# Kernel tuning notes

Measured on AMD Instinct MI355X. Metric: run time of the kernel, lower is better.

The kernel has to match this reference:

```python
import jax, jax.numpy as jnp
import numpy as np

N = 4096      # batch (e.g. nodes)
MUL = 128     # multiplicity of every irrep chunk
INV_SQRT3 = 1.0 / float(np.sqrt(3.0))  # CG norm for 1x1->0 and 0x1->1 / 1x0->1
INV_SQRT6 = 1.0 / float(np.sqrt(6.0))  # CG norm for 1x1->1 (Levi-Civita / sqrt(6))

# Levi-Civita tensor eps[i,j,k]
_EPS = np.zeros((3, 3, 3), dtype=np.float32)
for a, b, c in [(0, 1, 2), (1, 2, 0), (2, 0, 1)]:
    _EPS[a, b, c] = 1.0
    _EPS[a, c, b] = -1.0
EPS = jnp.asarray(_EPS)


def setup_inputs() -> dict:
    key = jax.random.key(0)
    ks = jax.random.split(key, 9)
    # e3nn path normalization folded into weight init std:
    # std = 1/sqrt(mul1*mul2*num_paths_into_that_output_irrep)
    std2 = 1.0 / float(np.sqrt(MUL * MUL * 2))  # scalar out: 2 paths
    std3 = 1.0 / float(np.sqrt(MUL * MUL * 3))  # vector out: 3 paths
    W = (MUL, MUL, MUL)
    return {
        "x1_s": jax.random.normal(ks[0], (N, MUL), dtype=jnp.float32),
        "x1_v": jax.random.normal(ks[1], (N, MUL, 3), dtype=jnp.float32),
        "x2_s": jax.random.normal(ks[2], (N, MUL), dtype=jnp.float32),
        "x2_v": jax.random.normal(ks[3], (N, MUL, 3), dtype=jnp.float32),
        "w_sss": jax.random.normal(ks[4], W, dtype=jnp.float32) * std2,
        "w_vvs": jax.random.normal(ks[5], W, dtype=jnp.float32) * std2,
        "w_svv": jax.random.normal(ks[6], W, dtype=jnp.float32) * std3,
        "w_vsv": jax.random.normal(ks[7], W, dtype=jnp.float32) * std3,
        "w_vvv": jax.random.normal(ks[8], W, dtype=jnp.float32) * std3,
    }


def reference(x1_s, x1_v, x2_s, x2_v, w_sss, w_vvs, w_svv, w_vsv, w_vvv):
    # ---- paths into 0e (scalar) output ----
    # 0e x 0e -> 0e : CG = 1
    a = jnp.einsum('nu,uvw->nvw', x1_s, w_sss)           # [N,MUL,MUL]
    out_s = jnp.einsum('nvw,nv->nw', a, x2_s)            # [N,MUL]
    # 1o x 1o -> 0e : CG = delta_ij / sqrt(3)
    dot = jnp.einsum('nui,nvi->nuv', x1_v, x2_v) * INV_SQRT3
    out_s = out_s + jnp.einsum('nuv,uvw->nw', dot, w_vvs)
    # ---- paths into 1o (vector) output ----
    # 0e x 1o -> 1o : CG = delta / sqrt(3)
    b = jnp.einsum('nu,uvw->nvw', x1_s, w_svv)
    out_v = jnp.einsum('nvw,nvk->nwk', b, x2_v) * INV_SQRT3   # [N,MUL,3]
    # 1o x 0e -> 1o : CG = delta / sqrt(3)
    c = jnp.einsum('nv,uvw->nuw', x2_s, w_vsv)
    out_v = out_v + jnp.einsum('nuw,nuk->nwk', c, x1_v) * INV_SQRT3
    # 1o x 1o -> 1o : CG = eps_ijk / sqrt(6)  (cross product)
    c1 = jnp.einsum('nvj,ijk->nvik', x2_v, EPS)               # [N,MUL,3,3]
    cross = jnp.einsum('nui,nvik->nuvk', x1_v, c1)            # [N,MUL,MUL,3]
    out_v = out_v + jnp.einsum('nuvk,uvw->nwk', cross, w_vvv) * INV_SQRT6
    # pack IrrepsArray 128x0e+128x1o as flat [N, 128 + 384]
    return jnp.concatenate([out_s, out_v.reshape(out_v.shape[0], -1)], axis=-1)
```

## Files before the change

### kernel.cpp

```cpp
#include <hip/hip_runtime.h>
#include <hip/hip_bf16.h>


typedef _Float16 f16;
typedef _Float16 f16x8 __attribute__((ext_vector_type(8)));
typedef _Float16 h2 __attribute__((ext_vector_type(2)));
typedef float f32x4 __attribute__((ext_vector_type(4)));
typedef unsigned u32;

#define WT_BYTES  (5u*4u*128u*4096u*2u)
#define X1_BYTES  (64u*4u*8192u*2u)
#define SLICE_EL  1310720u
#define CHUNK_EL  10240u

__device__ __forceinline__ h2 bc(u32 x){ union{u32 u; h2 h;} c; c.u=x; return c.h; }

union F8 { h2 h[4]; f16x8 v; };

__device__ __forceinline__ void gl_lds16(const f16* g, f16* l) {
    __builtin_amdgcn_global_load_lds(
        (const __attribute__((address_space(1))) void*)g,
        (__attribute__((address_space(3))) void*)l,
        16, 0, 0);
}

__global__ __launch_bounds__(256) void pack_w_kernel(
    const float* __restrict__ w0, const float* __restrict__ w1,
    const float* __restrict__ w2, const float* __restrict__ w3,
    const float* __restrict__ w4, f16* __restrict__ wt)
{
    __shared__ float tl[64][130];
    const int b = blockIdx.x;
    const int p = b >> 7;
    const int u = b & 127;
    const int usec = u >> 5;
    const int uin  = u & 31;
    const float* src = (p==0)?w0:(p==1)?w1:(p==2)?w2:(p==3)?w3:w4;
    const float scale = (p==0)?1.0f:(p==4)?0.40824829046386302f:0.57735026918962576f;

    for (int h = 0; h < 2; ++h) {
        const float* spR = src + (size_t)u*16384 + (size_t)h*8192;
        #pragma unroll
        for (int k = 0; k < 8; ++k) {
            const int e4 = (k*256 + threadIdx.x) * 4;
            const float4 v4 = *(const float4*)(spR + e4);
            const int vi = e4 >> 7, w = e4 & 127;
            tl[vi][w+0]=v4.x; tl[vi][w+1]=v4.y; tl[vi][w+2]=v4.z; tl[vi][w+3]=v4.w;
        }
        __syncthreads();
        #pragma unroll
        for (int k = 0; k < 4; ++k) {
            const int cid = k*256 + threadIdx.x;
            const int q     = cid & 3;
            const int wg    = (cid >> 2) & 127;
            const int vbh   = cid >> 9;
            const int vb    = h*2 + vbh;
            const int c     = vb*32 + uin;
            const int whalf = wg >> 6;
            const int wl    = wg & 63;
            const int qs    = q ^ ((wl >> 1) & 3);
            f16x8 t8;
            #pragma unroll
            for (int j = 0; j < 8; ++j)
                t8[j] = (f16)(tl[vbh*32 + q*8 + j][wg] * scale);
            *(f16x8*)(wt + (size_t)(usec*2 + whalf)*SLICE_EL + (size_t)c*CHUNK_EL
                          + p*2048 + wl*32 + qs*8) = t8;
        }
        __syncthreads();
    }
}

__global__ __launch_bounds__(256) void pack_x_kernel(
    const float* __restrict__ x1s, const float* __restrict__ x1v,
    const float* __restrict__ x2s, const float* __restrict__ x2v,
    f16* __restrict__ x1g, f16* __restrict__ x2g)
{
    if (blockIdx.x < 128) {
        __shared__ uint2 tl[128][33];
        const int nb = blockIdx.x;
        #pragma unroll
        for (int k = 0; k < 16; ++k) {
            const int idx = k*256 + threadIdx.x;
            const int u = idx & 127, nd = idx >> 7;
            const size_t i = (size_t)(nb*32 + nd)*128 + u;
            union { f16 h[4]; uint2 u2; } tp;
            tp.h[0] = (f16)x1s[i];
            tp.h[1] = (f16)x1v[i*3 + 0];
            tp.h[2] = (f16)x1v[i*3 + 1];
            tp.h[3] = (f16)x1v[i*3 + 2];
            tl[u][nd] = tp.u2;
        }
        __syncthreads();
        uint2* og = (uint2*)x1g;
        const int t = nb >> 1, nd0 = (nb & 1) * 32;
        #pragma unroll
        for (int k = 0; k < 16; ++k) {
            const int idx = k*256 + threadIdx.x;
            const int u = idx >> 5, nd = idx & 31;
            og[(((t*4 + (u>>5))*32 + (u&31)) << 6) + nd0 + nd] = tl[u][nd];
        }
    } else {
        const int tt = (blockIdx.x - 128)*256 + threadIdx.x;
        const int n = tt >> 7, v = tt & 127;
        const size_t b = (size_t)n*512;
        const size_t i = (size_t)n*128 + v;
        x2g[b +   0 + v] = (f16)x2s[i];
        x2g[b + 128 + v] = (f16)x2v[i*3 + 0];
        x2g[b + 256 + v] = (f16)x2v[i*3 + 1];
        x2g[b + 384 + v] = (f16)x2v[i*3 + 2];
    }
}

__global__ __launch_bounds__(256, 2) void tp_main(
    const f16* __restrict__ wt, const f16* __restrict__ x1g,
    const f16* __restrict__ x2g, float* __restrict__ out)
{
    __shared__ __align__(16) f16 wlds[2*CHUNK_EL];
    __shared__ __align__(16) f16 x1lds[8192];

    const int tid  = threadIdx.x;
    const int lane = tid & 63;
    const int wv   = tid >> 6;
    const int kg   = lane >> 4;
    const int lr   = lane & 15;

    const int b     = blockIdx.x;
    const int slice = b & 7;
    const int t     = b >> 3;
    const int usec  = slice >> 1;
    const int whalf = slice & 1;

    const f16* wstream = wt + (size_t)slice * SLICE_EL;

    int boff[4];
    #pragma unroll
    for (int ct = 0; ct < 4; ++ct) {
        const int wp = ct*16 + lr;
        boff[ct] = wp*32 + ((kg ^ ((wp >> 1) & 3)) * 8);
    }

    {
        const f16* src = x1g + ((size_t)(t*4 + usec) << 13);
        #pragma unroll
        for (int r = 0; r < 4; ++r)
            gl_lds16(src + r*2048 + wv*512 + lane*8, x1lds + r*2048 + wv*512 + lane*8);
    }
    #pragma unroll
    for (int r = 0; r < 5; ++r)
        gl_lds16(wstream + r*2048 + wv*512 + lane*8, wlds + r*2048 + wv*512 + lane*8);

    f32x4 acc[4][4];
    #pragma unroll
    for (int c2 = 0; c2 < 4; ++c2)
        #pragma unroll
        for (int d = 0; d < 4; ++d)
            acc[c2][d] = (f32x4){0.f, 0.f, 0.f, 0.f};

    h2 xq[4][4];
    const f16* wsrc = wstream + CHUNK_EL + wv*512 + lane*8;
    const f16* x2base = x2g + ((size_t)(t*64 + wv*16 + lr) << 9) + kg*8;
    const int nodel4 = (wv*16 + lr) * 4;

    for (int vb = 0; vb < 4; ++vb) {
        {
            const f16* xb = x2base + vb*32;
            uint4 h0 = *(const uint4*)(xb);
            uint4 h1 = *(const uint4*)(xb + 128);
            uint4 h2v = *(const uint4*)(xb + 256);
            uint4 h3 = *(const uint4*)(xb + 384);
            xq[0][0]=bc(h0.x); xq[0][1]=bc(h0.y); xq[0][2]=bc(h0.z); xq[0][3]=bc(h0.w);
            xq[1][0]=bc(h1.x); xq[1][1]=bc(h1.y); xq[1][2]=bc(h1.z); xq[1][3]=bc(h1.w);
            xq[2][0]=bc(h2v.x); xq[2][1]=bc(h2v.y); xq[2][2]=bc(h2v.z); xq[2][3]=bc(h2v.w);
            xq[3][0]=bc(h3.x); xq[3][1]=bc(h3.y); xq[3][2]=bc(h3.z); xq[3][3]=bc(h3.w);
        }
        for (int u2b = 0; u2b < 32; u2b += 2) {
            #pragma unroll
            for (int uu = 0; uu < 2; ++uu) {
                const int u2 = u2b + uu;
                const int c  = vb*32 + u2;

                asm volatile("s_waitcnt vmcnt(0)" ::: "memory");
                __builtin_amdgcn_s_barrier();
                __builtin_amdgcn_sched_barrier(0);

                if (c < 127) {
                    f16* dc = wlds + (uu^1)*CHUNK_EL + wv*512;
                    #pragma unroll
                    for (int r = 0; r < 5; ++r)
                        gl_lds16(wsrc + r*2048, dc + r*2048 + lane*8);
                }
                wsrc += CHUNK_EL;

                const uint2 h1 = *(const uint2*)(x1lds + u2*256 + nodel4);
                const h2 ps1 = bc(__builtin_amdgcn_perm(h1.x, h1.x, 0x01000100u));
                h2 pv[3];
                pv[0] = bc(__builtin_amdgcn_perm(h1.x, h1.x, 0x03020302u));
                pv[1] = bc(__builtin_amdgcn_perm(h1.y, h1.y, 0x01000100u));
                pv[2] = bc(__builtin_amdgcn_perm(h1.y, h1.y, 0x03020302u));

                F8 f0, f1, fa[3], fb[3], fc[3];
                #pragma unroll
                for (int j = 0; j < 4; ++j) {
                    f0.h[j] = ps1 * xq[0][j];
                    h2 d = pv[0] * xq[1][j];
                    d = __builtin_elementwise_fma(pv[1], xq[2][j], d);
                    f1.h[j] = __builtin_elementwise_fma(pv[2], xq[3][j], d);
                }
                #pragma unroll
                for (int k = 0; k < 3; ++k) {
                    const int k1 = (k+1) % 3, k2 = (k+2) % 3;
                    #pragma unroll
                    for (int j = 0; j < 4; ++j) {
                        fa[k].h[j] = ps1   * xq[1+k][j];
                        fb[k].h[j] = pv[k] * xq[0][j];
                        h2 tx = pv[k1] * xq[1+k2][j];
                        fc[k].h[j] = __builtin_elementwise_fma(-pv[k2], xq[1+k1][j], tx);
                    }
                }

                const f16* wb = wlds + uu*CHUNK_EL;
                #pragma unroll
                for (int ct = 0; ct < 4; ++ct) {
                    f16x8 b0 = *(const f16x8*)(wb +    0 + boff[ct]);
                    f16x8 b1 = *(const f16x8*)(wb + 2048 + boff[ct]);
                    f16x8 b2 = *(const f16x8*)(wb + 4096 + boff[ct]);
                    f16x8 b3 = *(const f16x8*)(wb + 6144 + boff[ct]);
                    f16x8 b4 = *(const f16x8*)(wb + 8192 + boff[ct]);
                    acc[ct][0] = __builtin_amdgcn_mfma_f32_16x16x32_f16(f0.v, b0, acc[ct][0], 0,0,0);
                    acc[ct][0] = __builtin_amdgcn_mfma_f32_16x16x32_f16(f1.v, b1, acc[ct][0], 0,0,0);
                    #pragma unroll
                    for (int k = 0; k < 3; ++k) {
                        acc[ct][1+k] = __builtin_amdgcn_mfma_f32_16x16x32_f16(fa[k].v, b2, acc[ct][1+k], 0,0,0);
                        acc[ct][1+k] = __builtin_amdgcn_mfma_f32_16x16x32_f16(fb[k].v, b3, acc[ct][1+k], 0,0,0);
                        acc[ct][1+k] = __builtin_amdgcn_mfma_f32_16x16x32_f16(fc[k].v, b4, acc[ct][1+k], 0,0,0);
                    }
                }
            }
        }
    }

    #pragma unroll
    for (int ct = 0; ct < 4; ++ct) {
        const int w = whalf*64 + ct*16 + lr;
        #pragma unroll
        for (int j = 0; j < 4; ++j) {
            const int n = t*64 + wv*16 + kg*4 + j;
            float* op = out + (size_t)n*512;
            unsafeAtomicAdd(op + w,             acc[ct][0][j]);
            unsafeAtomicAdd(op + 128 + w*3 + 0, acc[ct][1][j]);
            unsafeAtomicAdd(op + 128 + w*3 + 1, acc[ct][2][j]);
            unsafeAtomicAdd(op + 128 + w*3 + 2, acc[ct][3][j]);
        }
    }
}

extern "C" void kernel_launch(void* const* d_in, const int* in_sizes, int n_in,
                              void* d_out, int out_size, void* d_ws, size_t ws_size,
                              hipStream_t stream)
{
    const float* x1s = (const float*)d_in[0];
    const float* x1v = (const float*)d_in[1];
    const float* x2s = (const float*)d_in[2];
    const float* x2v = (const float*)d_in[3];
    const float* w0  = (const float*)d_in[4];
    const float* w1  = (const float*)d_in[5];
    const float* w2  = (const float*)d_in[6];
    const float* w3  = (const float*)d_in[7];
    const float* w4  = (const float*)d_in[8];

    f16* wtb = (f16*)d_ws;
    f16* x1g = (f16*)((char*)d_ws + WT_BYTES);
    f16* x2g = (f16*)((char*)d_ws + WT_BYTES + X1_BYTES);
    float* out = (float*)d_out;

    pack_w_kernel<<<640, 256, 0, stream>>>(w0, w1, w2, w3, w4, wtb);
    pack_x_kernel<<<2176, 256, 0, stream>>>(x1s, x1v, x2s, x2v, x1g, x2g);
    hipMemsetAsync(d_out, 0, (size_t)out_size*sizeof(float), stream);
    tp_main<<<512, 256, 0, stream>>>(wtb, x1g, x2g, out);
}
```

Measured before the change: 234.1 us.

## Double node tile per block to reuse each weight chunk across two row tiles

Each block now processes 128 nodes (two 16-row MFMA tiles per wave) instead of 64, so every streamed weight chunk loaded into LDS feeds twice as many MFMAs. The grid halves to 256 blocks and the x1 packing layout is widened to match. Weight streaming traffic from global/L2 is halved, at the cost of doubled accumulator registers (launch bounds reduced to one block per SM) and fewer blocks, which lowers occupancy and latency hiding. On a 256-CU part the 256 blocks give roughly one block per CU.

```diff
diff --git a/kernel.cpp b/kernel.cpp
--- a/kernel.cpp
+++ b/kernel.cpp
@@ -9,7 +9,7 @@
 typedef unsigned u32;
 
 #define WT_BYTES  (5u*4u*128u*4096u*2u)
-#define X1_BYTES  (64u*4u*8192u*2u)
+#define X1_BYTES  (32u*4u*16384u*2u)
 #define SLICE_EL  1310720u
 #define CHUNK_EL  10240u
 
@@ -92,12 +92,12 @@
         }
         __syncthreads();
         uint2* og = (uint2*)x1g;
-        const int t = nb >> 1, nd0 = (nb & 1) * 32;
+        const int t = nb >> 2, nd0 = (nb & 3) * 32;
         #pragma unroll
         for (int k = 0; k < 16; ++k) {
             const int idx = k*256 + threadIdx.x;
             const int u = idx >> 5, nd = idx & 31;
-            og[(((t*4 + (u>>5))*32 + (u&31)) << 6) + nd0 + nd] = tl[u][nd];
+            og[(((t*4 + (u>>5))*32 + (u&31)) << 7) + nd0 + nd] = tl[u][nd];
         }
     } else {
         const int tt = (blockIdx.x - 128)*256 + threadIdx.x;
@@ -111,12 +111,12 @@
     }
 }
 
-__global__ __launch_bounds__(256, 2) void tp_main(
+__global__ __launch_bounds__(256, 1) void tp_main(
     const f16* __restrict__ wt, const f16* __restrict__ x1g,
     const f16* __restrict__ x2g, float* __restrict__ out)
 {
     __shared__ __align__(16) f16 wlds[2*CHUNK_EL];
-    __shared__ __align__(16) f16 x1lds[8192];
+    __shared__ __align__(16) f16 x1lds[16384];
 
     const int tid  = threadIdx.x;
     const int lane = tid & 63;
@@ -140,38 +140,41 @@
     }
 
     {
-        const f16* src = x1g + ((size_t)(t*4 + usec) << 13);
-        #pragma unroll
-        for (int r = 0; r < 4; ++r)
-            gl_lds16(src + r*2048 + wv*512 + lane*8, x1lds + r*2048 + wv*512 + lane*8);
+        const f16* src = x1g + ((size_t)(t*4 + usec) << 14);
+        #pragma unroll
+        for (int r = 0; r < 8; ++r)
+            gl_lds16(src + r*2048 + tid*8, x1lds + r*2048 + tid*8);
     }
     #pragma unroll
     for (int r = 0; r < 5; ++r)
-        gl_lds16(wstream + r*2048 + wv*512 + lane*8, wlds + r*2048 + wv*512 + lane*8);
-
-    f32x4 acc[4][4];
-    #pragma unroll
-    for (int c2 = 0; c2 < 4; ++c2)
-        #pragma unroll
-        for (int d = 0; d < 4; ++d)
-            acc[c2][d] = (f32x4){0.f, 0.f, 0.f, 0.f};
-
-    h2 xq[4][4];
-    const f16* wsrc = wstream + CHUNK_EL + wv*512 + lane*8;
-    const f16* x2base = x2g + ((size_t)(t*64 + wv*16 + lr) << 9) + kg*8;
-    const int nodel4 = (wv*16 + lr) * 4;
+        gl_lds16(wstream + r*2048 + tid*8, wlds + r*2048 + tid*8);
+    __syncthreads();
+
+    f32x4 acc[2][4][4];
+    #pragma unroll
+    for (int rt = 0; rt < 2; ++rt)
+        #pragma unroll
+        for (int c2 = 0; c2 < 4; ++c2)
+            #pragma unroll
+            for (int d = 0; d < 4; ++d)
+                acc[rt][c2][d] = (f32x4){0.f, 0.f, 0.f, 0.f};
+
+    h2 xq[2][4][4];
+    const f16* wsrc = wstream + CHUNK_EL + tid*8;
 
     for (int vb = 0; vb < 4; ++vb) {
-        {
-            const f16* xb = x2base + vb*32;
-            uint4 h0 = *(const uint4*)(xb);
-            uint4 h1 = *(const uint4*)(xb + 128);
-            uint4 h2v = *(const uint4*)(xb + 256);
-            uint4 h3 = *(const uint4*)(xb + 384);
-            xq[0][0]=bc(h0.x); xq[0][1]=bc(h0.y); xq[0][2]=bc(h0.z); xq[0][3]=bc(h0.w);
-            xq[1][0]=bc(h1.x); xq[1][1]=bc(h1.y); xq[1][2]=bc(h1.z); xq[1][3]=bc(h1.w);
-            xq[2][0]=bc(h2v.x); xq[2][1]=bc(h2v.y); xq[2][2]=bc(h2v.z); xq[2][3]=bc(h2v.w);
-            xq[3][0]=bc(h3.x); xq[3][1]=bc(h3.y); xq[3][2]=bc(h3.z); xq[3][3]=bc(h3.w);
+        #pragma unroll
+        for (int rt = 0; rt < 2; ++rt) {
+            const int n = t*128 + wv*32 + rt*16 + lr;
+            const f16* xb = x2g + ((size_t)n << 9) + kg*8 + vb*32;
+            const uint4 h0 = *(const uint4*)(xb);
+            const uint4 h1 = *(const uint4*)(xb + 128);
+            const uint4 h2v = *(const uint4*)(xb + 256);
+            const uint4 h3 = *(const uint4*)(xb + 384);
+            xq[rt][0][0]=bc(h0.x); xq[rt][0][1]=bc(h0.y); xq[rt][0][2]=bc(h0.z); xq[rt][0][3]=bc(h0.w);
+            xq[rt][1][0]=bc(h1.x); xq[rt][1][1]=bc(h1.y); xq[rt][1][2]=bc(h1.z); xq[rt][1][3]=bc(h1.w);
+            xq[rt][2][0]=bc(h2v.x); xq[rt][2][1]=bc(h2v.y); xq[rt][2][2]=bc(h2v.z); xq[rt][2][3]=bc(h2v.w);
+            xq[rt][3][0]=bc(h3.x); xq[rt][3][1]=bc(h3.y); xq[rt][3][2]=bc(h3.z); xq[rt][3][3]=bc(h3.w);
         }
         for (int u2b = 0; u2b < 32; u2b += 2) {
             #pragma unroll
@@ -184,55 +187,60 @@
                 __builtin_amdgcn_sched_barrier(0);
 
                 if (c < 127) {
-                    f16* dc = wlds + (uu^1)*CHUNK_EL + wv*512;
+                    f16* dc = wlds + (uu^1)*CHUNK_EL + tid*8;
                     #pragma unroll
                     for (int r = 0; r < 5; ++r)
-                        gl_lds16(wsrc + r*2048, dc + r*2048 + lane*8);
+                        gl_lds16(wsrc + r*2048, dc + r*2048);
                 }
                 wsrc += CHUNK_EL;
 
-                const uint2 h1 = *(const uint2*)(x1lds + u2*256 + nodel4);
-                const h2 ps1 = bc(__builtin_amdgcn_perm(h1.x, h1.x, 0x01000100u));
-                h2 pv[3];
-                pv[0] = bc(__builtin_amdgcn_perm(h1.x, h1.x, 0x03020302u));
-                pv[1] = bc(__builtin_amdgcn_perm(h1.y, h1.y, 0x01000100u));
-                pv[2] = bc(__builtin_amdgcn_perm(h1.y, h1.y, 0x03020302u));
-
-                F8 f0, f1, fa[3], fb[3], fc[3];
+                F8 ag[2][11];
                 #pragma unroll
-                for (int j = 0; j < 4; ++j) {
-                    f0.h[j] = ps1 * xq[0][j];
-                    h2 d = pv[0] * xq[1][j];
-                    d = __builtin_elementwise_fma(pv[1], xq[2][j], d);
-                    f1.h[j] = __builtin_elementwise_fma(pv[2], xq[3][j], d);
-                }
-                #pragma unroll
-                for (int k = 0; k < 3; ++k) {
-                    const int k1 = (k+1) % 3, k2 = (k+2) % 3;
+                for (int rt = 0; rt < 2; ++rt) {
+                    const uint2 h1 = *(const uint2*)(x1lds + u2*512 + (wv*32 + rt*16 + lr)*4);
+                    const h2 ps1 = bc(__builtin_amdgcn_perm(h1.x, h1.x, 0x01000100u));
+                    h2 pv[3];
+                    pv[0] = bc(__builtin_amdgcn_perm(h1.x, h1.x, 0x03020302u));
+                    pv[1] = bc(__builtin_amdgcn_perm(h1.y, h1.y, 0x01000100u));
+                    pv[2] = bc(__builtin_amdgcn_perm(h1.y, h1.y, 0x03020302u));
                     #pragma unroll
                     for (int j = 0; j < 4; ++j) {
-                        fa[k].h[j] = ps1   * xq[1+k][j];
-                        fb[k].h[j] = pv[k] * xq[0][j];
-                        h2 tx = pv[k1] * xq[1+k2][j];
-                        fc[k].h[j] = __builtin_elementwise_fma(-pv[k2], xq[1+k1][j], tx);
+                        ag[rt][0].h[j] = ps1 * xq[rt][0][j];
+                        h2 d = pv[0] * xq[rt][1][j];
+                        d = __builtin_elementwise_fma(pv[1], xq[rt][2][j], d);
+                        ag[rt][1].h[j] = __builtin_elementwise_fma(pv[2], xq[rt][3][j], d);
+                    }
+                    #pragma unroll
+                    for (int k = 0; k < 3; ++k) {
+                        const int k1 = (k+1) % 3, k2 = (k+2) % 3;
+                        #pragma unroll
+                        for (int j = 0; j < 4; ++j) {
+                            ag[rt][2+k].h[j] = ps1   * xq[rt][1+k][j];
+                            ag[rt][5+k].h[j] = pv[k] * xq[rt][0][j];
+                            h2 tx = pv[k1] * xq[rt][1+k2][j];
+                            ag[rt][8+k].h[j] = __builtin_elementwise_fma(-pv[k2], xq[rt][1+k1][j], tx);
+                        }
                     }
                 }
 
                 const f16* wb = wlds + uu*CHUNK_EL;
                 #pragma unroll
                 for (int ct = 0; ct < 4; ++ct) {
-                    f16x8 b0 = *(const f16x8*)(wb +    0 + boff[ct]);
-                    f16x8 b1 = *(const f16x8*)(wb + 2048 + boff[ct]);
-                    f16x8 b2 = *(const f16x8*)(wb + 4096 + boff[ct]);
-                    f16x8 b3 = *(const f16x8*)(wb + 6144 + boff[ct]);
-                    f16x8 b4 = *(const f16x8*)(wb + 8192 + boff[ct]);
-                    acc[ct][0] = __builtin_amdgcn_mfma_f32_16x16x32_f16(f0.v, b0, acc[ct][0], 0,0,0);
-                    acc[ct][0] = __builtin_amdgcn_mfma_f32_16x16x32_f16(f1.v, b1, acc[ct][0], 0,0,0);
-                    #pragma unroll
-                    for (int k = 0; k < 3; ++k) {
-                        acc[ct][1+k] = __builtin_amdgcn_mfma_f32_16x16x32_f16(fa[k].v, b2, acc[ct][1+k], 0,0,0);
-                        acc[ct][1+k] = __builtin_amdgcn_mfma_f32_16x16x32_f16(fb[k].v, b3, acc[ct][1+k], 0,0,0);
-                        acc[ct][1+k] = __builtin_amdgcn_mfma_f32_16x16x32_f16(fc[k].v, b4, acc[ct][1+k], 0,0,0);
+                    const f16x8 b0 = *(const f16x8*)(wb +    0 + boff[ct]);
+                    const f16x8 b1 = *(const f16x8*)(wb + 2048 + boff[ct]);
+                    const f16x8 b2 = *(const f16x8*)(wb + 4096 + boff[ct]);
+                    const f16x8 b3 = *(const f16x8*)(wb + 6144 + boff[ct]);
+                    const f16x8 b4 = *(const f16x8*)(wb + 8192 + boff[ct]);
+                    #pragma unroll
+                    for (int rt = 0; rt < 2; ++rt) {
+                        acc[rt][ct][0] = __builtin_amdgcn_mfma_f32_16x16x32_f16(ag[rt][0].v, b0, acc[rt][ct][0], 0,0,0);
+                        acc[rt][ct][0] = __builtin_amdgcn_mfma_f32_16x16x32_f16(ag[rt][1].v, b1, acc[rt][ct][0], 0,0,0);
+                        #pragma unroll
+                        for (int k = 0; k < 3; ++k) {
+                            acc[rt][ct][1+k] = __builtin_amdgcn_mfma_f32_16x16x32_f16(ag[rt][2+k].v, b2, acc[rt][ct][1+k], 0,0,0);
+                            acc[rt][ct][1+k] = __builtin_amdgcn_mfma_f32_16x16x32_f16(ag[rt][5+k].v, b3, acc[rt][ct][1+k], 0,0,0);
+                            acc[rt][ct][1+k] = __builtin_amdgcn_mfma_f32_16x16x32_f16(ag[rt][8+k].v, b4, acc[rt][ct][1+k], 0,0,0);
+                        }
                     }
                 }
             }
@@ -240,16 +248,19 @@
     }
 
     #pragma unroll
-    for (int ct = 0; ct < 4; ++ct) {
-        const int w = whalf*64 + ct*16 + lr;
-        #pragma unroll
-        for (int j = 0; j < 4; ++j) {
-            const int n = t*64 + wv*16 + kg*4 + j;
-            float* op = out + (size_t)n*512;
-            unsafeAtomicAdd(op + w,             acc[ct][0][j]);
-            unsafeAtomicAdd(op + 128 + w*3 + 0, acc[ct][1][j]);
-            unsafeAtomicAdd(op + 128 + w*3 + 1, acc[ct][2][j]);
-            unsafeAtomicAdd(op + 128 + w*3 + 2, acc[ct][3][j]);
+    for (int rt = 0; rt < 2; ++rt) {
+        #pragma unroll
+        for (int ct = 0; ct < 4; ++ct) {
+            const int w = whalf*64 + ct*16 + lr;
+            #pragma unroll
+            for (int j = 0; j < 4; ++j) {
+                const int n = t*128 + wv*32 + rt*16 + kg*4 + j;
+                float* op = out + (size_t)n*512;
+                unsafeAtomicAdd(op + w,             acc[rt][ct][0][j]);
+                unsafeAtomicAdd(op + 128 + w*3 + 0, acc[rt][ct][1][j]);
+                unsafeAtomicAdd(op + 128 + w*3 + 1, acc[rt][ct][2][j]);
+                unsafeAtomicAdd(op + 128 + w*3 + 2, acc[rt][ct][3][j]);
+            }
         }
     }
 }
@@ -276,5 +287,5 @@
     pack_w_kernel<<<640, 256, 0, stream>>>(w0, w1, w2, w3, w4, wtb);
     pack_x_kernel<<<2176, 256, 0, stream>>>(x1s, x1v, x2s, x2v, x1g, x2g);
     hipMemsetAsync(d_out, 0, (size_t)out_size*sizeof(float), stream);
-    tp_main<<<512, 256, 0, stream>>>(wtb, x1g, x2g, out);
-}
+    tp_main<<<256, 256, 0, stream>>>(wtb, x1g, x2g, out);
+}
```

Measured after the change: 267.3 us. 1.14x slower.

## Triple-buffer weight chunks in LDS with partial vmcnt waits and MFMA priority

Applied to the files above, without the earlier changes.

Moves the weight stream from a double buffer to a triple LDS buffer, prefetching two chunks ahead and waiting only on the older chunk's loads (vmcnt(5)) instead of draining all loads each step. It also raises wave priority around the MFMA block with s_setprio. LDS use grows by one chunk (about 20 KB), which may cut the occupancy of two blocks per CU. An extra __syncthreads is added after the initial loads.

```diff
diff --git a/kernel.cpp b/kernel.cpp
--- a/kernel.cpp
+++ b/kernel.cpp
@@ -115,7 +115,7 @@
     const f16* __restrict__ wt, const f16* __restrict__ x1g,
     const f16* __restrict__ x2g, float* __restrict__ out)
 {
-    __shared__ __align__(16) f16 wlds[2*CHUNK_EL];
+    __shared__ __align__(16) f16 wlds[3*CHUNK_EL];
     __shared__ __align__(16) f16 x1lds[8192];
 
     const int tid  = threadIdx.x;
@@ -146,8 +146,12 @@
             gl_lds16(src + r*2048 + wv*512 + lane*8, x1lds + r*2048 + wv*512 + lane*8);
     }
     #pragma unroll
-    for (int r = 0; r < 5; ++r)
-        gl_lds16(wstream + r*2048 + wv*512 + lane*8, wlds + r*2048 + wv*512 + lane*8);
+    for (int k = 0; k < 2; ++k)
+        #pragma unroll
+        for (int r = 0; r < 5; ++r)
+            gl_lds16(wstream + k*CHUNK_EL + r*2048 + tid*8,
+                     wlds    + k*CHUNK_EL + r*2048 + tid*8);
+    __syncthreads();
 
     f32x4 acc[4][4];
     #pragma unroll
@@ -157,87 +161,93 @@
             acc[c2][d] = (f32x4){0.f, 0.f, 0.f, 0.f};
 
     h2 xq[4][4];
-    const f16* wsrc = wstream + CHUNK_EL + wv*512 + lane*8;
+    const f16* wsrc = wstream + 2*CHUNK_EL + tid*8;
     const f16* x2base = x2g + ((size_t)(t*64 + wv*16 + lr) << 9) + kg*8;
     const int nodel4 = (wv*16 + lr) * 4;
 
-    for (int vb = 0; vb < 4; ++vb) {
-        {
-            const f16* xb = x2base + vb*32;
-            uint4 h0 = *(const uint4*)(xb);
-            uint4 h1 = *(const uint4*)(xb + 128);
-            uint4 h2v = *(const uint4*)(xb + 256);
-            uint4 h3 = *(const uint4*)(xb + 384);
+    auto body = [&](int c, int bi) __attribute__((always_inline)) {
+        if ((c & 31) == 0) {
+            const f16* xb = x2base + (c >> 5)*32;
+            const uint4 h0 = *(const uint4*)(xb);
+            const uint4 h1 = *(const uint4*)(xb + 128);
+            const uint4 h2v = *(const uint4*)(xb + 256);
+            const uint4 h3 = *(const uint4*)(xb + 384);
             xq[0][0]=bc(h0.x); xq[0][1]=bc(h0.y); xq[0][2]=bc(h0.z); xq[0][3]=bc(h0.w);
             xq[1][0]=bc(h1.x); xq[1][1]=bc(h1.y); xq[1][2]=bc(h1.z); xq[1][3]=bc(h1.w);
             xq[2][0]=bc(h2v.x); xq[2][1]=bc(h2v.y); xq[2][2]=bc(h2v.z); xq[2][3]=bc(h2v.w);
             xq[3][0]=bc(h3.x); xq[3][1]=bc(h3.y); xq[3][2]=bc(h3.z); xq[3][3]=bc(h3.w);
         }
-        for (int u2b = 0; u2b < 32; u2b += 2) {
-            #pragma unroll
-            for (int uu = 0; uu < 2; ++uu) {
-                const int u2 = u2b + uu;
-                const int c  = vb*32 + u2;
-
-                asm volatile("s_waitcnt vmcnt(0)" ::: "memory");
-                __builtin_amdgcn_s_barrier();
-                __builtin_amdgcn_sched_barrier(0);
-
-                if (c < 127) {
-                    f16* dc = wlds + (uu^1)*CHUNK_EL + wv*512;
-                    #pragma unroll
-                    for (int r = 0; r < 5; ++r)
-                        gl_lds16(wsrc + r*2048, dc + r*2048 + lane*8);
-                }
-                wsrc += CHUNK_EL;
-
-                const uint2 h1 = *(const uint2*)(x1lds + u2*256 + nodel4);
-                const h2 ps1 = bc(__builtin_amdgcn_perm(h1.x, h1.x, 0x01000100u));
-                h2 pv[3];
-                pv[0] = bc(__builtin_amdgcn_perm(h1.x, h1.x, 0x03020302u));
-                pv[1] = bc(__builtin_amdgcn_perm(h1.y, h1.y, 0x01000100u));
-                pv[2] = bc(__builtin_amdgcn_perm(h1.y, h1.y, 0x03020302u));
-
-                F8 f0, f1, fa[3], fb[3], fc[3];
-                #pragma unroll
-                for (int j = 0; j < 4; ++j) {
-                    f0.h[j] = ps1 * xq[0][j];
-                    h2 d = pv[0] * xq[1][j];
-                    d = __builtin_elementwise_fma(pv[1], xq[2][j], d);
-                    f1.h[j] = __builtin_elementwise_fma(pv[2], xq[3][j], d);
-                }
-                #pragma unroll
-                for (int k = 0; k < 3; ++k) {
-                    const int k1 = (k+1) % 3, k2 = (k+2) % 3;
-                    #pragma unroll
-                    for (int j = 0; j < 4; ++j) {
-                        fa[k].h[j] = ps1   * xq[1+k][j];
-                        fb[k].h[j] = pv[k] * xq[0][j];
-                        h2 tx = pv[k1] * xq[1+k2][j];
-                        fc[k].h[j] = __builtin_elementwise_fma(-pv[k2], xq[1+k1][j], tx);
-                    }
-                }
-
-                const f16* wb = wlds + uu*CHUNK_EL;
-                #pragma unroll
-                for (int ct = 0; ct < 4; ++ct) {
-                    f16x8 b0 = *(const f16x8*)(wb +    0 + boff[ct]);
-                    f16x8 b1 = *(const f16x8*)(wb + 2048 + boff[ct]);
-                    f16x8 b2 = *(const f16x8*)(wb + 4096 + boff[ct]);
-                    f16x8 b3 = *(const f16x8*)(wb + 6144 + boff[ct]);
-                    f16x8 b4 = *(const f16x8*)(wb + 8192 + boff[ct]);
-                    acc[ct][0] = __builtin_amdgcn_mfma_f32_16x16x32_f16(f0.v, b0, acc[ct][0], 0,0,0);
-                    acc[ct][0] = __builtin_amdgcn_mfma_f32_16x16x32_f16(f1.v, b1, acc[ct][0], 0,0,0);
-                    #pragma unroll
-                    for (int k = 0; k < 3; ++k) {
-                        acc[ct][1+k] = __builtin_amdgcn_mfma_f32_16x16x32_f16(fa[k].v, b2, acc[ct][1+k], 0,0,0);
-                        acc[ct][1+k] = __builtin_amdgcn_mfma_f32_16x16x32_f16(fb[k].v, b3, acc[ct][1+k], 0,0,0);
-                        acc[ct][1+k] = __builtin_amdgcn_mfma_f32_16x16x32_f16(fc[k].v, b4, acc[ct][1+k], 0,0,0);
-                    }
-                }
+
+        if (c < 127) { asm volatile("s_waitcnt vmcnt(5)" ::: "memory"); }
+        else         { asm volatile("s_waitcnt vmcnt(0)" ::: "memory"); }
+        __builtin_amdgcn_s_barrier();
+        __builtin_amdgcn_sched_barrier(0);
+
+        if (c < 126) {
+            f16* dc = wlds + ((bi + 2) % 3)*CHUNK_EL + tid*8;
+            #pragma unroll
+            for (int r = 0; r < 5; ++r)
+                gl_lds16(wsrc + r*2048, dc + r*2048);
+        }
+        wsrc += CHUNK_EL;
+
+        const int u2 = c & 31;
+
+        const uint2 h1 = *(const uint2*)(x1lds + u2*256 + nodel4);
+        const h2 ps1 = bc(__builtin_amdgcn_perm(h1.x, h1.x, 0x01000100u));
+        h2 pv[3];
+        pv[0] = bc(__builtin_amdgcn_perm(h1.x, h1.x, 0x03020302u));
+        pv[1] = bc(__builtin_amdgcn_perm(h1.y, h1.y, 0x01000100u));
+        pv[2] = bc(__builtin_amdgcn_perm(h1.y, h1.y, 0x03020302u));
+
+        F8 f0, f1, fa[3], fb[3], fc[3];
+        #pragma unroll
+        for (int j = 0; j < 4; ++j) {
+            f0.h[j] = ps1 * xq[0][j];
+            h2 d = pv[0] * xq[1][j];
+            d = __builtin_elementwise_fma(pv[1], xq[2][j], d);
+            f1.h[j] = __builtin_elementwise_fma(pv[2], xq[3][j], d);
+        }
+        #pragma unroll
+        for (int k = 0; k < 3; ++k) {
+            const int k1 = (k+1) % 3, k2 = (k+2) % 3;
+            #pragma unroll
+            for (int j = 0; j < 4; ++j) {
+                fa[k].h[j] = ps1   * xq[1+k][j];
+                fb[k].h[j] = pv[k] * xq[0][j];
+                h2 tx = pv[k1] * xq[1+k2][j];
+                fc[k].h[j] = __builtin_elementwise_fma(-pv[k2], xq[1+k1][j], tx);
             }
         }
-    }
+
+        const f16* wb = wlds + bi*CHUNK_EL;
+        __builtin_amdgcn_s_setprio(1);
+        #pragma unroll
+        for (int ct = 0; ct < 4; ++ct) {
+            const f16x8 b0 = *(const f16x8*)(wb +    0 + boff[ct]);
+            const f16x8 b1 = *(const f16x8*)(wb + 2048 + boff[ct]);
+            const f16x8 b2 = *(const f16x8*)(wb + 4096 + boff[ct]);
+            const f16x8 b3 = *(const f16x8*)(wb + 6144 + boff[ct]);
+            const f16x8 b4 = *(const f16x8*)(wb + 8192 + boff[ct]);
+            acc[ct][0] = __builtin_amdgcn_mfma_f32_16x16x32_f16(f0.v, b0, acc[ct][0], 0,0,0);
+            acc[ct][0] = __builtin_amdgcn_mfma_f32_16x16x32_f16(f1.v, b1, acc[ct][0], 0,0,0);
+            #pragma unroll
+            for (int k = 0; k < 3; ++k) {
+                acc[ct][1+k] = __builtin_amdgcn_mfma_f32_16x16x32_f16(fa[k].v, b2, acc[ct][1+k], 0,0,0);
+                acc[ct][1+k] = __builtin_amdgcn_mfma_f32_16x16x32_f16(fb[k].v, b3, acc[ct][1+k], 0,0,0);
+                acc[ct][1+k] = __builtin_amdgcn_mfma_f32_16x16x32_f16(fc[k].v, b4, acc[ct][1+k], 0,0,0);
+            }
+        }
+        __builtin_amdgcn_s_setprio(0);
+    };
+
+    for (int cb = 0; cb < 126; cb += 3) {
+        body(cb + 0, 0);
+        body(cb + 1, 1);
+        body(cb + 2, 2);
+    }
+    body(126, 0);
+    body(127, 1);
 
     #pragma unroll
     for (int ct = 0; ct < 4; ++ct) {
```

Measured after the change: 240.2 us. +2.6%, slower.

## Switch to 32x32x16 MFMA tiles and stream weights directly into registers

Applied to the files above, without the earlier changes.

Replaces the 16x16x32 MFMA tiling with 32x32x16 tiles covering 128 nodes per block. Each block now handles 16 u-values per slice, across 16 slices. The LDS double-buffered weight stream, with its per-chunk barriers, is dropped; B fragments are loaded from global memory into registers with one-step software prefetch. The aim is to remove the barrier and LDS round-trip overhead and to reuse each B load across more rows. The cost is much higher register pressure from the B10 buffers and f32x16 accumulators, more global load traffic, and changed weight/x1 pack layouts. The launch grid must match the new 16-slice mapping, and that part of the host code is not shown.

```diff
diff --git a/kernel.cpp b/kernel.cpp
--- a/kernel.cpp
+++ b/kernel.cpp
@@ -5,17 +5,18 @@
 typedef _Float16 f16;
 typedef _Float16 f16x8 __attribute__((ext_vector_type(8)));
 typedef _Float16 h2 __attribute__((ext_vector_type(2)));
-typedef float f32x4 __attribute__((ext_vector_type(4)));
+typedef float f32x16 __attribute__((ext_vector_type(16)));
 typedef unsigned u32;
 
 #define WT_BYTES  (5u*4u*128u*4096u*2u)
-#define X1_BYTES  (64u*4u*8192u*2u)
-#define SLICE_EL  1310720u
+#define X1_BYTES  (32u*8u*8192u*2u)
+#define SLICE_EL  655360u
 #define CHUNK_EL  10240u
 
 __device__ __forceinline__ h2 bc(u32 x){ union{u32 u; h2 h;} c; c.u=x; return c.h; }
 
 union F8 { h2 h[4]; f16x8 v; };
+struct B10 { f16x8 v[10]; };
 
 __device__ __forceinline__ void gl_lds16(const f16* g, f16* l) {
     __builtin_amdgcn_global_load_lds(
@@ -33,8 +34,8 @@
     const int b = blockIdx.x;
     const int p = b >> 7;
     const int u = b & 127;
-    const int usec = u >> 5;
-    const int uin  = u & 31;
+    const int usec = u >> 4;
+    const int uin  = u & 15;
     const float* src = (p==0)?w0:(p==1)?w1:(p==2)?w2:(p==3)?w3:w4;
     const float scale = (p==0)?1.0f:(p==4)?0.40824829046386302f:0.57735026918962576f;
 
@@ -55,16 +56,18 @@
             const int wg    = (cid >> 2) & 127;
             const int vbh   = cid >> 9;
             const int vb    = h*2 + vbh;
-            const int c     = vb*32 + uin;
+            const int c     = vb*16 + uin;
+            const int kb    = q >> 1;
+            const int h2i   = q & 1;
             const int whalf = wg >> 6;
             const int wl    = wg & 63;
-            const int qs    = q ^ ((wl >> 1) & 3);
+            const int s     = usec*2 + whalf;
             f16x8 t8;
             #pragma unroll
             for (int j = 0; j < 8; ++j)
                 t8[j] = (f16)(tl[vbh*32 + q*8 + j][wg] * scale);
-            *(f16x8*)(wt + (size_t)(usec*2 + whalf)*SLICE_EL + (size_t)c*CHUNK_EL
-                          + p*2048 + wl*32 + qs*8) = t8;
+            *(f16x8*)(wt + (size_t)s*SLICE_EL + (size_t)c*CHUNK_EL
+                          + p*2048 + kb*1024 + wl*16 + h2i*8) = t8;
         }
         __syncthreads();
     }
@@ -92,12 +95,12 @@
         }
         __syncthreads();
         uint2* og = (uint2*)x1g;
-        const int t = nb >> 1, nd0 = (nb & 1) * 32;
+        const int t = nb >> 2, nd0 = (nb & 3) * 32;
         #pragma unroll
         for (int k = 0; k < 16; ++k) {
             const int idx = k*256 + threadIdx.x;
             const int u = idx >> 5, nd = idx & 31;
-            og[(((t*4 + (u>>5))*32 + (u&31)) << 6) + nd0 + nd] = tl[u][nd];
+            og[(((t*8 + (u>>4))*16 + (u&15)) << 7) + nd0 + nd] = tl[u][nd];
         }
     } else {
         const int tt = (blockIdx.x - 128)*256 + threadIdx.x;
@@ -111,145 +114,137 @@
     }
 }
 
+__device__ __forceinline__ B10 loadB(const f16* cb, int kb, int bo){
+    B10 r;
+    #pragma unroll
+    for (int p = 0; p < 5; ++p)
+        #pragma unroll
+        for (int ct = 0; ct < 2; ++ct)
+            r.v[p*2+ct] = *(const f16x8*)(cb + p*2048 + kb*1024 + ct*512 + bo);
+    return r;
+}
+
 __global__ __launch_bounds__(256, 2) void tp_main(
     const f16* __restrict__ wt, const f16* __restrict__ x1g,
     const f16* __restrict__ x2g, float* __restrict__ out)
 {
-    __shared__ __align__(16) f16 wlds[2*CHUNK_EL];
     __shared__ __align__(16) f16 x1lds[8192];
 
     const int tid  = threadIdx.x;
     const int lane = tid & 63;
     const int wv   = tid >> 6;
-    const int kg   = lane >> 4;
-    const int lr   = lane & 15;
+    const int l5   = lane & 31;
+    const int kg2  = lane >> 5;
 
     const int b     = blockIdx.x;
-    const int slice = b & 7;
-    const int t     = b >> 3;
+    const int slice = b & 15;
+    const int t     = b >> 4;
     const int usec  = slice >> 1;
     const int whalf = slice & 1;
 
-    const f16* wstream = wt + (size_t)slice * SLICE_EL;
-
-    int boff[4];
+    const f16* wbase = wt + (size_t)slice * SLICE_EL;
+    const int bo = l5*16 + kg2*8;
+
+    {
+        const f16* src = x1g + (size_t)(t*8 + usec) * 8192;
+        #pragma unroll
+        for (int r = 0; r < 4; ++r)
+            gl_lds16(src + r*2048 + tid*8, x1lds + r*2048 + tid*8);
+    }
+    __syncthreads();
+
+    f32x16 acc[2][4];
     #pragma unroll
-    for (int ct = 0; ct < 4; ++ct) {
-        const int wp = ct*16 + lr;
-        boff[ct] = wp*32 + ((kg ^ ((wp >> 1) & 3)) * 8);
-    }
-
-    {
-        const f16* src = x1g + ((size_t)(t*4 + usec) << 13);
-        #pragma unroll
-        for (int r = 0; r < 4; ++r)
-            gl_lds16(src + r*2048 + wv*512 + lane*8, x1lds + r*2048 + wv*512 + lane*8);
-    }
-    #pragma unroll
-    for (int r = 0; r < 5; ++r)
-        gl_lds16(wstream + r*2048 + wv*512 + lane*8, wlds + r*2048 + wv*512 + lane*8);
-
-    f32x4 acc[4][4];
-    #pragma unroll
-    for (int c2 = 0; c2 < 4; ++c2)
-        #pragma unroll
-        for (int d = 0; d < 4; ++d)
-            acc[c2][d] = (f32x4){0.f, 0.f, 0.f, 0.f};
-
-    h2 xq[4][4];
-    const f16* wsrc = wstream + CHUNK_EL + wv*512 + lane*8;
-    const f16* x2base = x2g + ((size_t)(t*64 + wv*16 + lr) << 9) + kg*8;
-    const int nodel4 = (wv*16 + lr) * 4;
-
-    for (int vb = 0; vb < 4; ++vb) {
-        {
-            const f16* xb = x2base + vb*32;
-            uint4 h0 = *(const uint4*)(xb);
-            uint4 h1 = *(const uint4*)(xb + 128);
-            uint4 h2v = *(const uint4*)(xb + 256);
-            uint4 h3 = *(const uint4*)(xb + 384);
-            xq[0][0]=bc(h0.x); xq[0][1]=bc(h0.y); xq[0][2]=bc(h0.z); xq[0][3]=bc(h0.w);
-            xq[1][0]=bc(h1.x); xq[1][1]=bc(h1.y); xq[1][2]=bc(h1.z); xq[1][3]=bc(h1.w);
-            xq[2][0]=bc(h2v.x); xq[2][1]=bc(h2v.y); xq[2][2]=bc(h2v.z); xq[2][3]=bc(h2v.w);
-            xq[3][0]=bc(h3.x); xq[3][1]=bc(h3.y); xq[3][2]=bc(h3.z); xq[3][3]=bc(h3.w);
-        }
-        for (int u2b = 0; u2b < 32; u2b += 2) {
-            #pragma unroll
-            for (int uu = 0; uu < 2; ++uu) {
-                const int u2 = u2b + uu;
-                const int c  = vb*32 + u2;
-
-                asm volatile("s_waitcnt vmcnt(0)" ::: "memory");
-                __builtin_amdgcn_s_barrier();
-                __builtin_amdgcn_sched_barrier(0);
-
-                if (c < 127) {
-                    f16* dc = wlds + (uu^1)*CHUNK_EL + wv*512;
-                    #pragma unroll
-                    for (int r = 0; r < 5; ++r)
-                        gl_lds16(wsrc + r*2048, dc + r*2048 + lane*8);
+    for (int c2 = 0; c2 < 2; ++c2)
+        #pragma unroll
+        for (int ch = 0; ch < 4; ++ch)
+            #pragma unroll
+            for (int r = 0; r < 16; ++r)
+                acc[c2][ch][r] = 0.f;
+
+    h2 xq[4][2][4];
+    const int node = wv*32 + l5;
+    const f16* x2b = x2g + (size_t)(t*128 + node)*512 + kg2*8;
+
+    const f16* cb = wbase;
+    B10 B0 = loadB(cb, 0, bo);
+    uint2 h1c = *(const uint2*)(x1lds + node*4);
+
+    for (int c = 0; c < 64; ++c) {
+        const int vb = c >> 4, u = c & 15;
+        if (u == 0) {
+            #pragma unroll
+            for (int q = 0; q < 4; ++q)
+                #pragma unroll
+                for (int kb = 0; kb < 2; ++kb) {
+                    const uint4 hx = *(const uint4*)(x2b + q*128 + vb*32 + kb*16);
+                    xq[q][kb][0]=bc(hx.x); xq[q][kb][1]=bc(hx.y);
+                    xq[q][kb][2]=bc(hx.z); xq[q][kb][3]=bc(hx.w);
                 }
-                wsrc += CHUNK_EL;
-
-                const uint2 h1 = *(const uint2*)(x1lds + u2*256 + nodel4);
-                const h2 ps1 = bc(__builtin_amdgcn_perm(h1.x, h1.x, 0x01000100u));
-                h2 pv[3];
-                pv[0] = bc(__builtin_amdgcn_perm(h1.x, h1.x, 0x03020302u));
-                pv[1] = bc(__builtin_amdgcn_perm(h1.y, h1.y, 0x01000100u));
-                pv[2] = bc(__builtin_amdgcn_perm(h1.y, h1.y, 0x03020302u));
-
-                F8 f0, f1, fa[3], fb[3], fc[3];
+        }
+        B10 B1 = loadB(cb, 1, bo);
+        const uint2 h1n = *(const uint2*)(x1lds + (((u+1)&15)*128 + node)*4);
+
+        const h2 ps1 = bc(__builtin_amdgcn_perm(h1c.x, h1c.x, 0x01000100u));
+        const h2 pv0 = bc(__builtin_amdgcn_perm(h1c.x, h1c.x, 0x03020302u));
+        const h2 pv1 = bc(__builtin_amdgcn_perm(h1c.y, h1c.y, 0x01000100u));
+        const h2 pv2 = bc(__builtin_amdgcn_perm(h1c.y, h1c.y, 0x03020302u));
+        const h2 pva[3] = {pv0, pv1, pv2};
+
+        auto compute = [&](int kb, const B10& BB) __attribute__((always_inline)) {
+            {
+                F8 f0, f1;
                 #pragma unroll
                 for (int j = 0; j < 4; ++j) {
-                    f0.h[j] = ps1 * xq[0][j];
-                    h2 d = pv[0] * xq[1][j];
-                    d = __builtin_elementwise_fma(pv[1], xq[2][j], d);
-                    f1.h[j] = __builtin_elementwise_fma(pv[2], xq[3][j], d);
+                    f0.h[j] = ps1 * xq[0][kb][j];
+                    h2 d = pv0 * xq[1][kb][j];
+                    d = __builtin_elementwise_fma(pv1, xq[2][kb][j], d);
+                    f1.h[j] = __builtin_elementwise_fma(pv2, xq[3][kb][j], d);
                 }
+                acc[0][0] = __builtin_amdgcn_mfma_f32_32x32x16_f16(f0.v, BB.v[0], acc[0][0], 0,0,0);
+                acc[1][0] = __builtin_amdgcn_mfma_f32_32x32x16_f16(f0.v, BB.v[1], acc[1][0], 0,0,0);
+                acc[0][0] = __builtin_amdgcn_mfma_f32_32x32x16_f16(f1.v, BB.v[2], acc[0][0], 0,0,0);
+                acc[1][0] = __builtin_amdgcn_mfma_f32_32x32x16_f16(f1.v, BB.v[3], acc[1][0], 0,0,0);
+            }
+            #pragma unroll
+            for (int k = 0; k < 3; ++k) {
+                const int k1 = (k+1) % 3, k2 = (k+2) % 3;
+                F8 fa, fb, fc;
                 #pragma unroll
-                for (int k = 0; k < 3; ++k) {
-                    const int k1 = (k+1) % 3, k2 = (k+2) % 3;
-                    #pragma unroll
-                    for (int j = 0; j < 4; ++j) {
-                        fa[k].h[j] = ps1   * xq[1+k][j];
-                        fb[k].h[j] = pv[k] * xq[0][j];
-                        h2 tx = pv[k1] * xq[1+k2][j];
-                        fc[k].h[j] = __builtin_elementwise_fma(-pv[k2], xq[1+k1][j], tx);
-                    }
+                for (int j = 0; j < 4; ++j) {
+                    fa.h[j] = ps1     * xq[1+k][kb][j];
+                    fb.h[j] = pva[k]  * xq[0][kb][j];
+                    h2 tx   = pva[k1] * xq[1+k2][kb][j];
+                    fc.h[j] = __builtin_elementwise_fma(-pva[k2], xq[1+k1][kb][j], tx);
                 }
-
-                const f16* wb = wlds + uu*CHUNK_EL;
-                #pragma unroll
-                for (int ct = 0; ct < 4; ++ct) {
-                    f16x8 b0 = *(const f16x8*)(wb +    0 + boff[ct]);
-                    f16x8 b1 = *(const f16x8*)(wb + 2048 + boff[ct]);
-                    f16x8 b2 = *(const f16x8*)(wb + 4096 + boff[ct]);
-                    f16x8 b3 = *(const f16x8*)(wb + 6144 + boff[ct]);
-                    f16x8 b4 = *(const f16x8*)(wb + 8192 + boff[ct]);
-                    acc[ct][0] = __builtin_amdgcn_mfma_f32_16x16x32_f16(f0.v, b0, acc[ct][0], 0,0,0);
-                    acc[ct][0] = __builtin_amdgcn_mfma_f32_16x16x32_f16(f1.v, b1, acc[ct][0], 0,0,0);
-                    #pragma unroll
-                    for (int k = 0; k < 3; ++k) {
-                        acc[ct][1+k] = __builtin_amdgcn_mfma_f32_16x16x32_f16(fa[k].v, b2, acc[ct][1+k], 0,0,0);
-                        acc[ct][1+k] = __builtin_amdgcn_mfma_f32_16x16x32_f16(fb[k].v, b3, acc[ct][1+k], 0,0,0);
-                        acc[ct][1+k] = __builtin_amdgcn_mfma_f32_16x16x32_f16(fc[k].v, b4, acc[ct][1+k], 0,0,0);
-                    }
-                }
+                acc[0][1+k] = __builtin_amdgcn_mfma_f32_32x32x16_f16(fa.v, BB.v[4], acc[0][1+k], 0,0,0);
+                acc[1][1+k] = __builtin_amdgcn_mfma_f32_32x32x16_f16(fa.v, BB.v[5], acc[1][1+k], 0,0,0);
+                acc[0][1+k] = __builtin_amdgcn_mfma_f32_32x32x16_f16(fb.v, BB.v[6], acc[0][1+k], 0,0,0);
+                acc[1][1+k] = __builtin_amdgcn_mfma_f32_32x32x16_f16(fb.v, BB.v[7], acc[1][1+k], 0,0,0);
+                acc[0][1+k] = __builtin_amdgcn_mfma_f32_32x32x16_f16(fc.v, BB.v[8], acc[0][1+k], 0,0,0);
+                acc[1][1+k] = __builtin_amdgcn_mfma_f32_32x32x16_f16(fc.v, BB.v[9], acc[1][1+k], 0,0,0);
             }
-        }
+        };
+
+        compute(0, B0);
+        B10 B0n = loadB(cb + CHUNK_EL, 0, bo);
+        compute(1, B1);
+        B0 = B0n;
+        h1c = h1n;
+        cb += CHUNK_EL;
     }
 
     #pragma unroll
-    for (int ct = 0; ct < 4; ++ct) {
-        const int w = whalf*64 + ct*16 + lr;
-        #pragma unroll
-        for (int j = 0; j < 4; ++j) {
-            const int n = t*64 + wv*16 + kg*4 + j;
+    for (int ct = 0; ct < 2; ++ct) {
+        const int w = whalf*64 + ct*32 + l5;
+        #pragma unroll
+        for (int r = 0; r < 16; ++r) {
+            const int n = t*128 + wv*32 + (r&3) + 8*(r>>2) + 4*kg2;
             float* op = out + (size_t)n*512;
-            unsafeAtomicAdd(op + w,             acc[ct][0][j]);
-            unsafeAtomicAdd(op + 128 + w*3 + 0, acc[ct][1][j]);
-            unsafeAtomicAdd(op + 128 + w*3 + 1, acc[ct][2][j]);
-            unsafeAtomicAdd(op + 128 + w*3 + 2, acc[ct][3][j]);
+            unsafeAtomicAdd(op + w,             acc[ct][0][r]);
+            unsafeAtomicAdd(op + 128 + w*3 + 0, acc[ct][1][r]);
+            unsafeAtomicAdd(op + 128 + w*3 + 1, acc[ct][2][r]);
+            unsafeAtomicAdd(op + 128 + w*3 + 2, acc[ct][3][r]);
         }
     }
 }
```

New measurement: 306.5 us. 1.31x slower.
